# Kernel tuning notes

Measured on AMD Instinct MI355X. Metric: run time of the kernel, lower is better.

Reference implementation:

```python
import jax, jax.numpy as jnp
import numpy as np
import math

B, S, H, NH = 2, 2048, 2048, 16
D = H // NH            # head dim = 128
FF = 4 * H
EPS = 1e-5


def layer_norm(x, w, b):
    mu = jnp.mean(x, axis=-1, keepdims=True)
    var = jnp.mean((x - mu) ** 2, axis=-1, keepdims=True)
    return (x - mu) * jax.lax.rsqrt(var + EPS) * w + b


def rotate_half(x):
    # split last dim into two halves (j=2 grouping), return (-x2, x1)
    x1, x2 = jnp.split(x, 2, axis=-1)
    return jnp.concatenate((-x2, x1), axis=-1)


def rope_freqs(seq_len, dim):
    inv_freq = 1.0 / (10000.0 ** (jnp.arange(0, dim, 2, dtype=jnp.float32) / dim))
    freqs = jnp.arange(seq_len, dtype=jnp.float32)[:, None] * inv_freq[None, :]
    return jnp.concatenate((freqs, freqs), axis=-1)  # [S, D]


def setup_inputs() -> dict:
    key = jax.random.key(0)
    ks = jax.random.split(key, 8)
    sc_h = 1.0 / math.sqrt(H)
    sc_ff = 1.0 / math.sqrt(FF)
    return {
        "hidden_states": jax.random.normal(ks[0], (B, S, H), jnp.float32),
        "attention_mask": jnp.zeros((1, 1, S, S), jnp.bool_),
        "ln1_w": jnp.ones((H,), jnp.float32),
        "ln1_b": jnp.zeros((H,), jnp.float32),
        "wqkv": jax.random.uniform(ks[1], (3 * H, H), jnp.float32, -sc_h, sc_h),
        "bqkv": jnp.zeros((3 * H,), jnp.float32),
        "wdense": jax.random.uniform(ks[2], (H, H), jnp.float32, -sc_h, sc_h),
        "bdense": jnp.zeros((H,), jnp.float32),
        "ln2_w": jnp.ones((H,), jnp.float32),
        "ln2_b": jnp.zeros((H,), jnp.float32),
        "w1": jax.random.uniform(ks[3], (FF, H), jnp.float32, -sc_h, sc_h),
        "b1": jnp.zeros((FF,), jnp.float32),
        "w2": jax.random.uniform(ks[4], (H, FF), jnp.float32, -sc_ff, sc_ff),
        "b2": jnp.zeros((H,), jnp.float32),
    }


def reference(hidden_states, attention_mask, ln1_w, ln1_b, wqkv, bqkv,
              wdense, bdense, ln2_w, ln2_b, w1, b1, w2, b2):
    residual = hidden_states
    x = layer_norm(hidden_states, ln1_w, ln1_b)

    qkv = jnp.einsum('bsh,oh->bso', x, wqkv) + bqkv           # [B,S,3H]
    qkv = qkv.reshape(B, S, NH, 3 * D).transpose(0, 2, 1, 3)  # [B,NH,S,3D]
    q, k, v = jnp.split(qkv, 3, axis=-1)                      # each [B,NH,S,D]

    pos = rope_freqs(S, D)                                    # [S,D]
    cos, sin = jnp.cos(pos), jnp.sin(pos)
    q = q * cos + rotate_half(q) * sin
    k = k * cos + rotate_half(k) * sin

    scale = 1.0 / math.sqrt(D)
    scores = jnp.einsum('bhqd,bhkd->bhqk', q, k) * scale      # [B,NH,S,S]
    causal = jnp.tril(jnp.ones((S, S), jnp.bool_))
    scores = jnp.where(causal, scores.astype(jnp.float32), -1e9)
    probs = jax.nn.softmax(scores, axis=-1).astype(v.dtype)

    ctx = jnp.einsum('bhqk,bhkd->bhqd', probs, v)             # [B,NH,S,D]
    ctx = ctx.transpose(0, 2, 1, 3).reshape(B, S, H)
    attn_out = jnp.einsum('bsh,oh->bso', ctx, wdense) + bdense

    hidden = residual + attn_out
    residual = hidden
    x = layer_norm(hidden, ln2_w, ln2_b)
    inter = jax.nn.gelu(jnp.einsum('bsh,fh->bsf', x, w1) + b1, approximate=False)
    out = jnp.einsum('bsf,hf->bsh', inter, w2) + b2
    hidden = residual + out
    return (hidden, attention_mask)
```

## Files before the change

kernel.cpp:

```cpp
#include <hip/hip_runtime.h>
#include <math.h>

typedef unsigned short u16;
typedef unsigned int u32;
typedef __attribute__((ext_vector_type(8))) __bf16 bf16x8;
typedef __attribute__((ext_vector_type(4))) float f32x4;
typedef __attribute__((ext_vector_type(8))) u16 u16x8;
typedef __attribute__((ext_vector_type(4))) u16 u16x4;

#define BB 2
#define SS 2048
#define HH 2048
#define NHH 16
#define DD 128
#define FFF 8192
#define MM (BB * SS)

__device__ __forceinline__ u16 f2bf(float f) {
  u32 u = __float_as_uint(f);
  u32 r = (u + 0x7FFFu + ((u >> 16) & 1u)) >> 16;
  return (u16)r;
}
__device__ __forceinline__ float b2f(u16 h) {
  return __uint_as_float(((u32)h) << 16);
}
__device__ __forceinline__ void gll16(const void* g, void* l) {
  __builtin_amdgcn_global_load_lds((const __attribute__((address_space(1))) void*)g,
                                   (__attribute__((address_space(3))) void*)l, 16, 0, 0);
}

struct CvtArgs {
  const float* src[4];
  u16* dst[4];
  int n[4];
};
__global__ __launch_bounds__(256) void cvt_all(CvtArgs a) {
  const int seg = blockIdx.y;
  const int i = (blockIdx.x * 256 + threadIdx.x) * 4;
  if (i + 3 < a.n[seg]) {
    f32x4 v = *(const f32x4*)(a.src[seg] + i);
    u16x4 o;
    o[0] = f2bf(v[0]); o[1] = f2bf(v[1]); o[2] = f2bf(v[2]); o[3] = f2bf(v[3]);
    *(u16x4*)(a.dst[seg] + i) = o;
  }
}

__global__ __launch_bounds__(256) void ln_bf16(const float* __restrict__ x,
                                               const float* __restrict__ w,
                                               const float* __restrict__ bsh,
                                               u16* __restrict__ out) {
  const int row = blockIdx.x, tid = threadIdx.x;
  const float* xr = x + (size_t)row * HH;
  f32x4 a = ((const f32x4*)xr)[tid * 2];
  f32x4 b = ((const f32x4*)xr)[tid * 2 + 1];
  float s = a[0] + a[1] + a[2] + a[3] + b[0] + b[1] + b[2] + b[3];
  float q = a[0]*a[0] + a[1]*a[1] + a[2]*a[2] + a[3]*a[3]
          + b[0]*b[0] + b[1]*b[1] + b[2]*b[2] + b[3]*b[3];
#pragma unroll
  for (int off = 32; off > 0; off >>= 1) {
    s += __shfl_down(s, off);
    q += __shfl_down(q, off);
  }
  __shared__ float red[8];
  const int wave = tid >> 6;
  if ((tid & 63) == 0) { red[wave] = s; red[4 + wave] = q; }
  __syncthreads();
  s = red[0] + red[1] + red[2] + red[3];
  q = red[4] + red[5] + red[6] + red[7];
  const float mean = s * (1.0f / HH);
  const float var = q * (1.0f / HH) - mean * mean;
  const float rstd = 1.0f / sqrtf(var + 1e-5f);
  f32x4 w0 = ((const f32x4*)w)[tid * 2];
  f32x4 w1 = ((const f32x4*)w)[tid * 2 + 1];
  f32x4 b0 = ((const f32x4*)bsh)[tid * 2];
  f32x4 b1 = ((const f32x4*)bsh)[tid * 2 + 1];
  u16x8 o;
#pragma unroll
  for (int i = 0; i < 4; ++i) o[i] = f2bf((a[i] - mean) * rstd * w0[i] + b0[i]);
#pragma unroll
  for (int i = 0; i < 4; ++i) o[4 + i] = f2bf((b[i] - mean) * rstd * w1[i] + b1[i]);
  *(u16x8*)(out + (size_t)row * HH + tid * 8) = o;
}

template <int MODE, int DB>
__global__ __launch_bounds__(256) void gemm_bt(const u16* __restrict__ A,
                                               const u16* __restrict__ Bw,
                                               const float* __restrict__ bias,
                                               const float* resid, void* Cout,
                                               int M, int N, int K) {
  __shared__ __align__(16) u16 As[DB ? 2 : 1][128 * 64];
  __shared__ __align__(16) u16 Bs[DB ? 2 : 1][128 * 64];
  const int tid = threadIdx.x;
  const int wave = tid >> 6, lane = tid & 63;
  const int l15 = lane & 15, quad = lane >> 4;
  const int bm = blockIdx.x, bn = blockIdx.y;
  const int wm = (wave >> 1) << 6, wn = (wave & 1) << 6;

  f32x4 acc[4][4] = {};

  const int srow = (wave << 5) + (lane >> 3);
  const int sg = (lane & 7) ^ (lane >> 3);
  const u16* aptr = A + (size_t)(bm * 128 + srow) * K + sg * 8;
  const u16* bptr = Bw + (size_t)(bn * 128 + srow) * K + sg * 8;

  auto stage = [&](int buf) {
#pragma unroll
    for (int i = 0; i < 4; ++i)
      gll16(aptr + (size_t)i * 8 * K, &As[buf][(wave * 4 + i) * 512]);
#pragma unroll
    for (int i = 0; i < 4; ++i)
      gll16(bptr + (size_t)i * 8 * K, &Bs[buf][(wave * 4 + i) * 512]);
    aptr += 64; bptr += 64;
  };

  auto compute = [&](int buf) {
#pragma unroll
    for (int tt = 0; tt < 2; ++tt) {
      bf16x8 af[4], bfv[4];
#pragma unroll
      for (int i = 0; i < 4; ++i) {
        const int m = wm + i * 16 + l15;
        const int n = wn + i * 16 + l15;
        const int gi = tt * 4 + quad;
        af[i] = *(const bf16x8*)&As[buf][m * 64 + ((gi ^ (m & 7)) << 3)];
        bfv[i] = *(const bf16x8*)&Bs[buf][n * 64 + ((gi ^ (n & 7)) << 3)];
      }
#pragma unroll
      for (int i = 0; i < 4; ++i)
#pragma unroll
        for (int j = 0; j < 4; ++j)
          acc[i][j] = __builtin_amdgcn_mfma_f32_16x16x32_bf16(af[i], bfv[j], acc[i][j], 0, 0, 0);
    }
  };

  const int nk = K >> 6;
  if constexpr (DB) {
    stage(0);
    for (int kt = 0; kt < nk; ++kt) {
      __syncthreads();
      if (kt + 1 < nk) stage((kt + 1) & 1);
      compute(kt & 1);
    }
  } else {
    for (int kt = 0; kt < nk; ++kt) {
      stage(0);
      __syncthreads();
      compute(0);
      __syncthreads();
    }
  }

#pragma unroll
  for (int i = 0; i < 4; ++i) {
    const int row0 = bm * 128 + wm + i * 16 + quad * 4;
#pragma unroll
    for (int j = 0; j < 4; ++j) {
      const int col = bn * 128 + wn + j * 16 + l15;
      const float bv = bias[col];
#pragma unroll
      for (int r = 0; r < 4; ++r) {
        const size_t idx = (size_t)(row0 + r) * N + col;
        float v = acc[i][j][r] + bv;
        if constexpr (MODE == 0) {
          ((u16*)Cout)[idx] = f2bf(v);
        } else if constexpr (MODE == 1) {
          ((float*)Cout)[idx] = v + resid[idx];
        } else {
          v = 0.5f * v * (1.0f + erff(v * 0.70710678118654752f));
          ((u16*)Cout)[idx] = f2bf(v);
        }
      }
    }
  }
}

template <int MODE>
__global__ __launch_bounds__(512, 2) void gemm256(const u16* __restrict__ A,
                                                  const u16* __restrict__ Bw,
                                                  const float* __restrict__ bias,
                                                  void* Cout, int M, int N, int K) {
  __shared__ __align__(16) u16 As[2][256 * 64];
  __shared__ __align__(16) u16 Bs[2][256 * 64];
  const int tid = threadIdx.x;
  const int wave = tid >> 6, lane = tid & 63;
  const int l15 = lane & 15, quad = lane >> 4;
  const int wm = wave >> 2, wn = wave & 3;
  const int bm = blockIdx.x, bn = blockIdx.y;

  f32x4 acc[8][4] = {};

  const size_t loff = (size_t)(lane >> 3) * K + (size_t)(((lane & 7) ^ (lane >> 3)) << 3);
  const u16* Abase = A + (size_t)(bm * 256) * K + loff;
  const u16* Bbase = Bw + (size_t)(bn * 256) * K + loff;

  auto stageA = [&](int buf, int kt, int h) {
#pragma unroll
    for (int i = 0; i < 2; ++i) {
      const int c = wave * 2 + i;
      const int rb = ((c & 8) << 4) | (h * 64 + (c & 7) * 8);
      gll16(Abase + (size_t)rb * K + kt * 64, &As[buf][rb * 64]);
    }
  };
  auto stageB = [&](int buf, int kt, int h) {
#pragma unroll
    for (int i = 0; i < 2; ++i) {
      const int c = wave * 2 + i;
      const int rb = (c >> 2) * 64 + h * 32 + (c & 3) * 8;
      gll16(Bbase + (size_t)rb * K + kt * 64, &Bs[buf][rb * 64]);
    }
  };

  auto ldA = [&](const u16* as_, int qm, bf16x8 (&dst)[4][2]) {
#pragma unroll
    for (int im = 0; im < 4; ++im) {
      const int ar = wm * 128 + qm * 64 + im * 16 + l15;
#pragma unroll
      for (int tt = 0; tt < 2; ++tt)
        dst[im][tt] = *(const bf16x8*)&as_[ar * 64 + ((((tt << 2) + quad) ^ (ar & 7)) << 3)];
    }
  };
  auto ldB = [&](const u16* bs_, int qn, bf16x8 (&dst)[2][2]) {
#pragma unroll
    for (int jn = 0; jn < 2; ++jn) {
      const int br = wn * 64 + qn * 32 + jn * 16 + l15;
#pragma unroll
      for (int tt = 0; tt < 2; ++tt)
        dst[jn][tt] = *(const bf16x8*)&bs_[br * 64 + ((((tt << 2) + quad) ^ (br & 7)) << 3)];
    }
  };
  auto mm = [&](bf16x8 (&a)[4][2], bf16x8 (&b)[2][2], int i0, int j0) {
    __builtin_amdgcn_s_setprio(1);
#pragma unroll
    for (int tt = 0; tt < 2; ++tt)
#pragma unroll
      for (int im = 0; im < 4; ++im)
#pragma unroll
        for (int jn = 0; jn < 2; ++jn)
          acc[i0 + im][j0 + jn] = __builtin_amdgcn_mfma_f32_16x16x32_bf16(
              a[im][tt], b[jn][tt], acc[i0 + im][j0 + jn], 0, 0, 0);
    __builtin_amdgcn_s_setprio(0);
  };

#define BAR256() __builtin_amdgcn_s_barrier()

  const u16* const As0 = As[0];
  const u16* const As1 = As[1];
  const u16* const Bs0 = Bs[0];
  const u16* const Bs1 = Bs[1];

  const int nk = K >> 6;
  const int niter = nk >> 1;

  stageA(0, 0, 0); stageB(0, 0, 0); stageA(0, 0, 1); stageB(0, 0, 1);
  stageA(1, 1, 0); stageB(1, 1, 0); stageA(1, 1, 1);
  asm volatile("s_waitcnt vmcnt(6)" ::: "memory");
  BAR256();

  for (int it = 0; it < niter; ++it) {
    const int t0 = it * 2, t1 = t0 + 1;
    const bool pf = (t0 + 2 < nk);
    bf16x8 a0[4][2], a1[4][2], b0[2][2], b1[2][2];

    ldA(As0, 0, a0); ldB(Bs0, 0, b0);
    stageB(1, t1, 1);
    BAR256();
    mm(a0, b0, 0, 0);
    BAR256();
    ldA(As0, 1, a1);
    if (pf) stageA(0, t0 + 2, 0);
    BAR256();
    mm(a1, b0, 4, 0);
    BAR256();
    ldB(Bs0, 1, b1);
    if (pf) stageB(0, t0 + 2, 0);
    BAR256();
    mm(a1, b1, 4, 2);
    BAR256();
    if (pf) stageA(0, t0 + 2, 1);
    BAR256();
    mm(a0, b1, 0, 2);
    if (pf) asm volatile("s_waitcnt vmcnt(6)" ::: "memory");
    else    asm volatile("s_waitcnt vmcnt(0)" ::: "memory");
    BAR256();

    ldA(As1, 0, a0); ldB(Bs1, 0, b0);
    if (pf) stageB(0, t0 + 2, 1);
    BAR256();
    mm(a0, b0, 0, 0);
    BAR256();
    ldA(As1, 1, a1);
    if (pf) stageA(1, t1 + 2, 0);
    BAR256();
    mm(a1, b0, 4, 0);
    BAR256();
    ldB(Bs1, 1, b1);
    if (pf) stageB(1, t1 + 2, 0);
    BAR256();
    mm(a1, b1, 4, 2);
    BAR256();
    if (pf) stageA(1, t1 + 2, 1);
    BAR256();
    mm(a0, b1, 0, 2);
    if (pf) asm volatile("s_waitcnt vmcnt(6)" ::: "memory");
    else    asm volatile("s_waitcnt vmcnt(0)" ::: "memory");
    BAR256();
  }
#undef BAR256

#pragma unroll
  for (int i = 0; i < 8; ++i) {
    const int row0 = bm * 256 + wm * 128 + i * 16 + quad * 4;
#pragma unroll
    for (int j = 0; j < 4; ++j) {
      const int col = bn * 256 + wn * 64 + j * 16 + l15;
      const float bv = bias[col];
#pragma unroll
      for (int r = 0; r < 4; ++r) {
        const size_t idx = (size_t)(row0 + r) * N + col;
        float v = acc[i][j][r] + bv;
        if constexpr (MODE == 0) {
          ((u16*)Cout)[idx] = f2bf(v);
        } else {
          v = 0.5f * v * (1.0f + erff(v * 0.70710678118654752f));
          ((u16*)Cout)[idx] = f2bf(v);
        }
      }
    }
  }
}

__global__ __launch_bounds__(256) void rope_kernel(const u16* __restrict__ qkv,
                                                   u16* __restrict__ Qr,
                                                   u16* __restrict__ Kr) {
  const int tid = threadIdx.x;
  const int d = tid & 63;
  const int s = blockIdx.x * 4 + (tid >> 6);
  const int h = blockIdx.y, b = blockIdx.z;
  const u16* row = qkv + ((size_t)(b * SS + s)) * (3 * HH) + h * (3 * DD);
  const float q1 = b2f(row[d]),        q2 = b2f(row[d + 64]);
  const float k1 = b2f(row[DD + d]),   k2 = b2f(row[DD + d + 64]);
  const float inv = expf((float)d * -0.14391156830963714f);
  const float ang = (float)s * inv;
  const float cs = cosf(ang), sn = sinf(ang);
  const size_t o = ((size_t)(b * NHH + h) * SS + s) * DD;
  Qr[o + d]      = f2bf(q1 * cs - q2 * sn);
  Qr[o + d + 64] = f2bf(q2 * cs + q1 * sn);
  Kr[o + d]      = f2bf(k1 * cs - k2 * sn);
  Kr[o + d + 64] = f2bf(k2 * cs + k1 * sn);
}

__device__ __forceinline__ int vslot(int s, int chunk) {
  return chunk ^ (s & 7) ^ ((s >> 3) & 7);
}
__global__ __launch_bounds__(256) void vtrans(const u16* __restrict__ qkv,
                                              u16* __restrict__ Vt) {
  __shared__ __align__(16) u16 Vs[64 * 128];
  const int tid = threadIdx.x;
  const int s0 = blockIdx.x * 64;
  const int bh = blockIdx.y;
  const int b = bh >> 4, h = bh & 15;
  const u16* src = qkv + (size_t)(b * SS + s0) * (3 * HH) + h * (3 * DD) + 2 * DD;
#pragma unroll
  for (int rr = 0; rr < 4; ++rr) {
    const int task = tid + rr * 256;
    const int sr = task >> 4, c = task & 15;
    u16x8 v = *(const u16x8*)(src + (size_t)sr * (3 * HH) + c * 8);
    const int sl = (vslot(sr, c & 7) | (c & 8));
    *(u16x8*)&Vs[sr * 128 + sl * 8] = v;
  }
  __syncthreads();
#pragma unroll
  for (int rr = 0; rr < 4; ++rr) {
    const int task = tid + rr * 256;
    const int dr = task >> 3, c = task & 7;
    u16x8 o;
#pragma unroll
    for (int e = 0; e < 8; ++e) {
      const int s = c * 8 + e;
      const int sl = (vslot(s, dr >> 3 & 7) | ((dr >> 3) & 8));
      o[e] = Vs[s * 128 + sl * 8 + (dr & 7)];
    }
    *(u16x8*)(Vt + (size_t)(bh * DD + dr) * SS + s0 + c * 8) = o;
  }
}

__device__ __forceinline__ void softmax_pv(f32x4 s4[4], bool diag, int qrl0,
                                           float m_run[4], float l_run[4],
                                           f32x4 oacc[8], const u16* vtb,
                                           u16* psw, int quad, int l15) {
  const float SCL = 0.12751742904630190f;
  float pv[4][4];
  float mx[4] = {-3e38f, -3e38f, -3e38f, -3e38f};
#pragma unroll
  for (int jt = 0; jt < 4; ++jt)
#pragma unroll
    for (int r = 0; r < 4; ++r) {
      float sv = s4[jt][r] * SCL;
      if (diag && (jt * 16 + l15) > (qrl0 + r)) sv = -3e38f;
      pv[jt][r] = sv;
      mx[r] = fmaxf(mx[r], sv);
    }
#pragma unroll
  for (int r = 0; r < 4; ++r) {
    mx[r] = fmaxf(mx[r], __shfl_xor(mx[r], 1));
    mx[r] = fmaxf(mx[r], __shfl_xor(mx[r], 2));
    mx[r] = fmaxf(mx[r], __shfl_xor(mx[r], 4));
    mx[r] = fmaxf(mx[r], __shfl_xor(mx[r], 8));
  }
  float al[4];
#pragma unroll
  for (int r = 0; r < 4; ++r) {
    const float mnew = fmaxf(m_run[r], mx[r]);
    al[r] = exp2f(m_run[r] - mnew);
    m_run[r] = mnew;
  }
  float rs[4] = {0.f, 0.f, 0.f, 0.f};
#pragma unroll
  for (int jt = 0; jt < 4; ++jt)
#pragma unroll
    for (int r = 0; r < 4; ++r) {
      const float pp = exp2f(pv[jt][r] - m_run[r]);
      pv[jt][r] = pp;
      rs[r] += pp;
    }
#pragma unroll
  for (int r = 0; r < 4; ++r) {
    rs[r] += __shfl_xor(rs[r], 1);
    rs[r] += __shfl_xor(rs[r], 2);
    rs[r] += __shfl_xor(rs[r], 4);
    rs[r] += __shfl_xor(rs[r], 8);
    l_run[r] = l_run[r] * al[r] + rs[r];
  }
#pragma unroll
  for (int jn = 0; jn < 8; ++jn)
#pragma unroll
    for (int r = 0; r < 4; ++r) oacc[jn][r] *= al[r];
#pragma unroll
  for (int jt = 0; jt < 4; ++jt)
#pragma unroll
    for (int r = 0; r < 4; ++r) {
      const int qr = quad * 4 + r, key = jt * 16 + l15;
      psw[qr * 64 + (((key >> 3) ^ (qr & 7)) << 3) + (key & 7)] = f2bf(pv[jt][r]);
    }
  __threadfence_block();
#pragma unroll
  for (int t = 0; t < 2; ++t) {
    const int gg = t * 4 + quad;
    bf16x8 pf = *(const bf16x8*)&psw[l15 * 64 + ((gg ^ (l15 & 7)) << 3)];
#pragma unroll
    for (int jn = 0; jn < 8; ++jn) {
      const int nd = jn * 16 + l15;
      bf16x8 vf = *(const bf16x8*)&vtb[nd * 64 + ((gg ^ (nd & 7)) << 3)];
      oacc[jn] = __builtin_amdgcn_mfma_f32_16x16x32_bf16(pf, vf, oacc[jn], 0, 0, 0);
    }
  }
}

__global__ __launch_bounds__(256, 2) void attn_kernel(const u16* __restrict__ Q,
                                                      const u16* __restrict__ Kg,
                                                      const u16* __restrict__ Vtg,
                                                      u16* __restrict__ ctx) {
  __shared__ __align__(16) u16 Ks[2][64 * 128];
  __shared__ __align__(16) u16 Vt[2][128 * 64];
  __shared__ __align__(16) u16 Ps[4][16 * 64];
  const int tid = threadIdx.x;
  const int wave = tid >> 6, lane = tid & 63;
  const int l15 = lane & 15, quad = lane >> 4;
  const int p = blockIdx.x, h = blockIdx.y, b = blockIdx.z;
  const int qlo = p, qhi = 31 - p;
  const size_t bh = (size_t)(b * NHH + h);
  const u16* Qp = Q + bh * ((size_t)SS * DD);
  const u16* Kp = Kg + bh * ((size_t)SS * DD);
  const u16* Vp = Vtg + bh * ((size_t)DD * SS);

  bf16x8 qfl[4], qfh[4];
  {
    const u16* ql = Qp + (size_t)(qlo * 64 + wave * 16 + l15) * DD + quad * 8;
    const u16* qh = Qp + (size_t)(qhi * 64 + wave * 16 + l15) * DD + quad * 8;
#pragma unroll
    for (int t = 0; t < 4; ++t) {
      qfl[t] = *(const bf16x8*)(ql + t * 32);
      qfh[t] = *(const bf16x8*)(qh + t * 32);
    }
  }

  f32x4 oal[8] = {}, oah[8] = {};
  float ml[4] = {-3e38f, -3e38f, -3e38f, -3e38f};
  float mh[4] = {-3e38f, -3e38f, -3e38f, -3e38f};
  float ll[4] = {0.f, 0.f, 0.f, 0.f}, lh[4] = {0.f, 0.f, 0.f, 0.f};

  auto stage = [&](int kt, int bufi) {
    const int k0 = kt * 64;
#pragma unroll
    for (int i = 0; i < 4; ++i) {
      const int g = wave * 4 + i;
      const int r = g * 4 + quad;
      const int c = l15 ^ (r & 15);
      gll16(Kp + (size_t)(k0 + r) * DD + c * 8, &Ks[bufi][g * 512]);
    }
#pragma unroll
    for (int i = 0; i < 4; ++i) {
      const int g = wave * 4 + i;
      const int d = g * 8 + (lane >> 3);
      const int c = (lane & 7) ^ (d & 7);
      gll16(Vp + (size_t)d * SS + k0 + c * 8, &Vt[bufi][g * 512]);
    }
  };

  stage(0, 0);
  const int qrl0 = wave * 16 + quad * 4;
  for (int kt = 0; kt <= qhi; ++kt) {
    __syncthreads();
    const u16* ksb = Ks[kt & 1];
    const u16* vtb = Vt[kt & 1];
    if (kt < qhi) stage(kt + 1, (kt + 1) & 1);
    const bool lo = (kt <= qlo);

    f32x4 sh4[4] = {}, sl4[4] = {};
#pragma unroll
    for (int t = 0; t < 4; ++t)
#pragma unroll
      for (int jt = 0; jt < 4; ++jt) {
        const int key = jt * 16 + l15;
        bf16x8 kf = *(const bf16x8*)&ksb[key * 128 + (((t * 4 + quad) ^ (key & 15)) << 3)];
        sh4[jt] = __builtin_amdgcn_mfma_f32_16x16x32_bf16(qfh[t], kf, sh4[jt], 0, 0, 0);
        if (lo) sl4[jt] = __builtin_amdgcn_mfma_f32_16x16x32_bf16(qfl[t], kf, sl4[jt], 0, 0, 0);
      }

    softmax_pv(sh4, kt == qhi, qrl0, mh, lh, oah, vtb, Ps[wave], quad, l15);
    if (lo) softmax_pv(sl4, kt == qlo, qrl0, ml, ll, oal, vtb, Ps[wave], quad, l15);
  }

  float invh[4], invl[4];
#pragma unroll
  for (int r = 0; r < 4; ++r) { invh[r] = 1.0f / lh[r]; invl[r] = 1.0f / ll[r]; }
#pragma unroll
  for (int jn = 0; jn < 8; ++jn)
#pragma unroll
    for (int r = 0; r < 4; ++r) {
      const int col = h * DD + jn * 16 + l15;
      const int rh = qhi * 64 + qrl0 + r;
      const int rl = qlo * 64 + qrl0 + r;
      ctx[(size_t)(b * SS + rh) * HH + col] = f2bf(oah[jn][r] * invh[r]);
      ctx[(size_t)(b * SS + rl) * HH + col] = f2bf(oal[jn][r] * invl[r]);
    }
}

extern "C" void kernel_launch(void* const* d_in, const int* in_sizes, int n_in,
                              void* d_out, int out_size, void* d_ws, size_t ws_size,
                              hipStream_t stream) {
  (void)in_sizes; (void)n_in; (void)ws_size;
  const float* hidden = (const float*)d_in[0];
  const float* ln1w = (const float*)d_in[2];
  const float* ln1b = (const float*)d_in[3];
  const float* wqkv = (const float*)d_in[4];
  const float* bqkv = (const float*)d_in[5];
  const float* wdense = (const float*)d_in[6];
  const float* bdense = (const float*)d_in[7];
  const float* ln2w = (const float*)d_in[8];
  const float* ln2b = (const float*)d_in[9];
  const float* w1 = (const float*)d_in[10];
  const float* b1 = (const float*)d_in[11];
  const float* w2 = (const float*)d_in[12];
  const float* b2 = (const float*)d_in[13];

  char* ws = (char*)d_ws;
  size_t off = 0;
  auto alloc = [&](size_t elems) {
    u16* p = (u16*)(ws + off);
    off += ((elems * 2 + 255) & ~(size_t)255);
    return p;
  };
  u16* wqkvbf = alloc((size_t)3 * HH * HH);
  u16* wdbf   = alloc((size_t)HH * HH);
  u16* w1bf   = alloc((size_t)FFF * HH);
  u16* w2bf   = alloc((size_t)HH * FFF);
  u16* xbf    = alloc((size_t)MM * HH);
  u16* ctx    = alloc((size_t)MM * HH);
  u16* big    = alloc((size_t)MM * 3 * HH + 3 * (size_t)BB * NHH * SS * DD);
  u16* qkvbuf = big;
  u16* Qr = big + (size_t)MM * 3 * HH;
  u16* Kr = Qr + (size_t)BB * NHH * SS * DD;
  u16* Vtg = Kr + (size_t)BB * NHH * SS * DD;
  u16* inter = big;

  CvtArgs ca;
  ca.src[0] = wqkv;   ca.dst[0] = wqkvbf; ca.n[0] = 3 * HH * HH;
  ca.src[1] = wdense; ca.dst[1] = wdbf;   ca.n[1] = HH * HH;
  ca.src[2] = w1;     ca.dst[2] = w1bf;   ca.n[2] = FFF * HH;
  ca.src[3] = w2;     ca.dst[3] = w2bf;   ca.n[3] = HH * FFF;
  cvt_all<<<dim3((FFF * HH) / 1024, 4), 256, 0, stream>>>(ca);

  ln_bf16<<<MM, 256, 0, stream>>>(hidden, ln1w, ln1b, xbf);
  gemm256<0><<<dim3(MM / 256, (3 * HH) / 256), 512, 0, stream>>>(
      xbf, wqkvbf, bqkv, qkvbuf, MM, 3 * HH, HH);
  rope_kernel<<<dim3(SS / 4, NHH, BB), 256, 0, stream>>>(qkvbuf, Qr, Kr);
  vtrans<<<dim3(SS / 64, BB * NHH), 256, 0, stream>>>(qkvbuf, Vtg);
  attn_kernel<<<dim3(16, NHH, BB), 256, 0, stream>>>(Qr, Kr, Vtg, ctx);
  gemm_bt<1, 1><<<dim3(MM / 128, HH / 128), 256, 0, stream>>>(
      ctx, wdbf, bdense, hidden, d_out, MM, HH, HH);
  ln_bf16<<<MM, 256, 0, stream>>>((const float*)d_out, ln2w, ln2b, xbf);
  gemm256<2><<<dim3(MM / 256, FFF / 256), 512, 0, stream>>>(
      xbf, w1bf, b1, inter, MM, FFF, HH);
  gemm_bt<1, 1><<<dim3(MM / 128, HH / 128), 256, 0, stream>>>(
      inter, w2bf, b2, (const float*)d_out, d_out, MM, HH, FFF);

  const size_t hid_elems = (size_t)MM * HH;
  if ((size_t)out_size > hid_elems)
    hipMemsetAsync((char*)d_out + hid_elems * 4, 0,
                   ((size_t)out_size - hid_elems) * 4, stream);
}
```

Before: 920.4 us.

## Flatten weight conversion grid, vectorize RoPE, use 128-tile GEMM for QKV

The weight conversion kernel now uses a flat 1D grid with segment lookup, so no blocks are launched idle for the smaller weight matrices. RoPE processes two adjacent elements per thread with 32-bit loads and stores, halving the thread count. The QKV projection switches from the 256-tile, 512-thread GEMM to the 128-tile gemm_bt path, trading per-block reuse for more blocks. The QKV GEMM swap could be slower if the larger tile was more efficient.

Result: no change. 925.4 us (+0.6%).

```diff
diff --git a/kernel.cpp b/kernel.cpp
--- a/kernel.cpp
+++ b/kernel.cpp
@@ -32,17 +32,19 @@
 struct CvtArgs {
   const float* src[4];
   u16* dst[4];
-  int n[4];
 };
 __global__ __launch_bounds__(256) void cvt_all(CvtArgs a) {
-  const int seg = blockIdx.y;
-  const int i = (blockIdx.x * 256 + threadIdx.x) * 4;
-  if (i + 3 < a.n[seg]) {
-    f32x4 v = *(const f32x4*)(a.src[seg] + i);
-    u16x4 o;
-    o[0] = f2bf(v[0]); o[1] = f2bf(v[1]); o[2] = f2bf(v[2]); o[3] = f2bf(v[3]);
-    *(u16x4*)(a.dst[seg] + i) = o;
-  }
+  const int fi = blockIdx.x * 256 + threadIdx.x;
+  int seg, base;
+  if (fi < 3145728)      { seg = 0; base = 0; }
+  else if (fi < 4194304) { seg = 1; base = 3145728; }
+  else if (fi < 8388608) { seg = 2; base = 4194304; }
+  else                   { seg = 3; base = 8388608; }
+  const int i = (fi - base) * 4;
+  f32x4 v = *(const f32x4*)(a.src[seg] + i);
+  u16x4 o;
+  o[0] = f2bf(v[0]); o[1] = f2bf(v[1]); o[2] = f2bf(v[2]); o[3] = f2bf(v[3]);
+  *(u16x4*)(a.dst[seg] + i) = o;
 }
 
 __global__ __launch_bounds__(256) void ln_bf16(const float* __restrict__ x,
@@ -333,20 +335,30 @@
                                                    u16* __restrict__ Qr,
                                                    u16* __restrict__ Kr) {
   const int tid = threadIdx.x;
-  const int d = tid & 63;
-  const int s = blockIdx.x * 4 + (tid >> 6);
+  const int j = tid & 31;
+  const int s = blockIdx.x * 8 + (tid >> 5);
   const int h = blockIdx.y, b = blockIdx.z;
   const u16* row = qkv + ((size_t)(b * SS + s)) * (3 * HH) + h * (3 * DD);
-  const float q1 = b2f(row[d]),        q2 = b2f(row[d + 64]);
-  const float k1 = b2f(row[DD + d]),   k2 = b2f(row[DD + d + 64]);
-  const float inv = expf((float)d * -0.14391156830963714f);
-  const float ang = (float)s * inv;
-  const float cs = cosf(ang), sn = sinf(ang);
+  const u32 qlo = *(const u32*)(row + 2 * j);
+  const u32 qhi = *(const u32*)(row + 64 + 2 * j);
+  const u32 klo = *(const u32*)(row + DD + 2 * j);
+  const u32 khi = *(const u32*)(row + DD + 64 + 2 * j);
+  const float c = -0.14391156830963714f;
+  const float inv0 = expf((float)(2 * j) * c);
+  const float inv1 = expf((float)(2 * j + 1) * c);
+  const float a0 = (float)s * inv0, a1 = (float)s * inv1;
+  const float cs0 = cosf(a0), sn0 = sinf(a0);
+  const float cs1 = cosf(a1), sn1 = sinf(a1);
+  const float q10 = b2f((u16)qlo), q11 = b2f((u16)(qlo >> 16));
+  const float q20 = b2f((u16)qhi), q21 = b2f((u16)(qhi >> 16));
+  const float k10 = b2f((u16)klo), k11 = b2f((u16)(klo >> 16));
+  const float k20 = b2f((u16)khi), k21 = b2f((u16)(khi >> 16));
   const size_t o = ((size_t)(b * NHH + h) * SS + s) * DD;
-  Qr[o + d]      = f2bf(q1 * cs - q2 * sn);
-  Qr[o + d + 64] = f2bf(q2 * cs + q1 * sn);
-  Kr[o + d]      = f2bf(k1 * cs - k2 * sn);
-  Kr[o + d + 64] = f2bf(k2 * cs + k1 * sn);
+  auto pk = [](float x, float y) { return (u32)f2bf(x) | ((u32)f2bf(y) << 16); };
+  *(u32*)(Qr + o + 2 * j)      = pk(q10 * cs0 - q20 * sn0, q11 * cs1 - q21 * sn1);
+  *(u32*)(Qr + o + 64 + 2 * j) = pk(q20 * cs0 + q10 * sn0, q21 * cs1 + q11 * sn1);
+  *(u32*)(Kr + o + 2 * j)      = pk(k10 * cs0 - k20 * sn0, k11 * cs1 - k21 * sn1);
+  *(u32*)(Kr + o + 64 + 2 * j) = pk(k20 * cs0 + k10 * sn0, k21 * cs1 + k11 * sn1);
 }
 
 __device__ __forceinline__ int vslot(int s, int chunk) {
@@ -585,16 +597,16 @@
   u16* inter = big;
 
   CvtArgs ca;
-  ca.src[0] = wqkv;   ca.dst[0] = wqkvbf; ca.n[0] = 3 * HH * HH;
-  ca.src[1] = wdense; ca.dst[1] = wdbf;   ca.n[1] = HH * HH;
-  ca.src[2] = w1;     ca.dst[2] = w1bf;   ca.n[2] = FFF * HH;
-  ca.src[3] = w2;     ca.dst[3] = w2bf;   ca.n[3] = HH * FFF;
-  cvt_all<<<dim3((FFF * HH) / 1024, 4), 256, 0, stream>>>(ca);
+  ca.src[0] = wqkv;   ca.dst[0] = wqkvbf;
+  ca.src[1] = wdense; ca.dst[1] = wdbf;
+  ca.src[2] = w1;     ca.dst[2] = w1bf;
+  ca.src[3] = w2;     ca.dst[3] = w2bf;
+  cvt_all<<<49152, 256, 0, stream>>>(ca);
 
   ln_bf16<<<MM, 256, 0, stream>>>(hidden, ln1w, ln1b, xbf);
-  gemm256<0><<<dim3(MM / 256, (3 * HH) / 256), 512, 0, stream>>>(
-      xbf, wqkvbf, bqkv, qkvbuf, MM, 3 * HH, HH);
-  rope_kernel<<<dim3(SS / 4, NHH, BB), 256, 0, stream>>>(qkvbuf, Qr, Kr);
+  gemm_bt<0, 0><<<dim3(MM / 128, (3 * HH) / 128), 256, 0, stream>>>(
+      xbf, wqkvbf, bqkv, nullptr, qkvbuf, MM, 3 * HH, HH);
+  rope_kernel<<<dim3(SS / 8, NHH, BB), 256, 0, stream>>>(qkvbuf, Qr, Kr);
   vtrans<<<dim3(SS / 64, BB * NHH), 256, 0, stream>>>(qkvbuf, Vtg);
   attn_kernel<<<dim3(16, NHH, BB), 256, 0, stream>>>(Qr, Kr, Vtg, ctx);
   gemm_bt<1, 1><<<dim3(MM / 128, HH / 128), 256, 0, stream>>>(
```
